# Kernel tuning notes

Hardware: AMD Instinct MI355X
Metric: run time of the kernel (lower is better)

Reference implementation:

```python
import jax, jax.numpy as jnp
import numpy as np

B, S, F_ATT, R, A = 1024, 96, 2048, 512, 512  # batch, att_size, att_feat_size, rnn_size, att_hid_size

def setup_inputs() -> dict:
    key = jax.random.key(0)
    ks = jax.random.split(key, 16)
    def lin(k, out_d, in_d):
        s = 1.0 / np.sqrt(in_d)
        kw, kb = jax.random.split(k)
        return (jax.random.uniform(kw, (out_d, in_d), jnp.float32, -s, s),
                jax.random.uniform(kb, (out_d,), jnp.float32, -s, s))
    W_ae, b_ae = lin(ks[0], R, F_ATT)   # att_embed Linear
    W_c,  b_c  = lin(ks[1], A, R)       # ctx2att
    W_s,  b_s  = lin(ks[2], A, R)       # sentinel_embed
    W_h,  b_h  = lin(ks[3], A, R)       # ho_embed
    W_al, b_al = lin(ks[4], 1, A)       # alpha_net
    W_o,  b_o  = lin(ks[5], R, R)       # att2h
    return {
        'h': jax.random.normal(ks[6], (B, R), jnp.float32),
        'sentinel': jax.random.normal(ks[7], (B, R), jnp.float32),
        'att_feats': jax.random.normal(ks[8], (B, S, F_ATT), jnp.float32),
        'W_ae': W_ae, 'b_ae': b_ae, 'W_c': W_c, 'b_c': b_c,
        'W_s': W_s, 'b_s': b_s, 'W_h': W_h, 'b_h': b_h,
        'W_al': W_al, 'b_al': b_al, 'W_o': W_o, 'b_o': b_o,
    }

def reference(h, sentinel, att_feats, W_ae, b_ae, W_c, b_c, W_s, b_s,
              W_h, b_h, W_al, b_al, W_o, b_o):
    # att_embed: Linear(2048->512) + ReLU (dropout = identity in eval)
    att = jax.nn.relu(jnp.einsum('bsf,rf->bsr', att_feats, W_ae) + b_ae)  # [B,S,R]
    att_embd = jnp.einsum('bsr,ar->bsa', att, W_c) + b_c                   # [B,S,A]
    sent_e = sentinel @ W_s.T + b_s                                        # [B,A]
    h_e = h @ W_h.T + b_h                                                  # [B,A]
    # concat sentinel slot in front of attention features
    img_all = jnp.concatenate([sentinel[:, None, :], att], axis=1)         # [B,S+1,R]
    img_all_embed = jnp.concatenate([sent_e[:, None, :], att_embd], axis=1)  # [B,S+1,A]
    hA = jnp.tanh(img_all_embed + h_e[:, None, :])                         # [B,S+1,A]
    logits = jnp.einsum('bsa,a->bs', hA, W_al[0]) + b_al[0]                # [B,S+1]
    alpha = jax.nn.softmax(logits, axis=-1)
    cHat = jnp.einsum('bs,bsr->br', alpha, img_all)                        # [B,R]
    atten_out = cHat + h
    return jnp.tanh(atten_out @ W_o.T + b_o)                               # [B,R]
```

## Files before the change

### kernel.cpp

```cpp
#include <hip/hip_runtime.h>

#define M1 98304
#define RDIM 512
#define FDIM 2048
#define SDIM 96
#define BM 96
#define BK 64

typedef __attribute__((ext_vector_type(8))) __bf16 bf16x8;
typedef __attribute__((ext_vector_type(4))) float f32x4;

#define WAITV6 asm volatile("s_waitcnt vmcnt(6)" ::: "memory")
#define WAITV3 asm volatile("s_waitcnt vmcnt(3)" ::: "memory")
#define WAITV0 asm volatile("s_waitcnt vmcnt(0)" ::: "memory")
#define WAITL0 asm volatile("s_waitcnt lgkmcnt(0)" ::: "memory")
#define SBAR   __builtin_amdgcn_s_barrier()
#define SCHED0 __builtin_amdgcn_sched_barrier(0)

__device__ __forceinline__ float bf2f(unsigned short u){
  union { unsigned int i; float f; } v; v.i = ((unsigned int)u) << 16; return v.f;
}
__device__ __forceinline__ unsigned short f2bf(float f){
  union { float f; unsigned int i; } v; v.f = f;
  unsigned int r = v.i + 0x7FFFu + ((v.i >> 16) & 1u);
  return (unsigned short)(r >> 16);
}
__device__ __forceinline__ unsigned short f2bfn(float f){
  __bf16 b = (__bf16)f;
  return __builtin_bit_cast(unsigned short, b);
}
__device__ __forceinline__ float fast_tanh(float x){
  float e = __expf(2.f * x);
  return 1.f - 2.f / (e + 1.f);
}
__device__ __forceinline__ void gld_lds16(const void* g, void* l){
  __builtin_amdgcn_global_load_lds((const __attribute__((address_space(1))) void*)g,
                                   (__attribute__((address_space(3))) void*)l, 16, 0, 0);
}
__device__ __forceinline__ f32x4 mfma16(bf16x8 a, bf16x8 b, f32x4 c){
  return __builtin_amdgcn_mfma_f32_16x16x32_bf16(a, b, c, 0, 0, 0);
}

__device__ __forceinline__ void cat_store_a(const float* __restrict__ src,
                                            unsigned short* __restrict__ dst, int idx){
  float x = src[idx];
  int r = idx >> 9, c = idx & 511;
  unsigned short hi = f2bf(x);
  unsigned short lo = f2bf(x - bf2f(hi));
  unsigned short* p = dst + (long)r * 1536 + c;
  p[0] = hi; p[512] = lo; p[1024] = hi;
}
__device__ __forceinline__ void cat_store_w(const float* __restrict__ src,
                                            unsigned short* __restrict__ dst, int idx){
  float x = src[idx];
  int r = idx >> 9, c = idx & 511;
  unsigned short hi = f2bf(x);
  unsigned short lo = f2bf(x - bf2f(hi));
  unsigned short* p = dst + (long)r * 1536 + c;
  p[0] = hi; p[512] = hi; p[1024] = lo;
}

__global__ void k_convert(const float* W_ae, const float* W_c, const float* W_s,
                          const float* W_h, const float* W_o,
                          const float* h, const float* sent,
                          unsigned short* W_ae_bf, unsigned short* W_c_bf,
                          unsigned short* W_s_cat, unsigned short* W_h_cat,
                          unsigned short* W_o_cat, unsigned short* h_cat,
                          unsigned short* s_cat){
  const int stride = 1024 * 256;
  int i0 = blockIdx.x * 256 + threadIdx.x;
  switch (blockIdx.y) {
    case 0: for (int i = i0; i < 512*2048; i += stride) W_ae_bf[i] = f2bf(W_ae[i]); break;
    case 1: for (int i = i0; i < 512*512;  i += stride) W_c_bf[i]  = f2bf(W_c[i]);  break;
    case 2: for (int i = i0; i < 512*512;  i += stride) cat_store_w(W_s, W_s_cat, i); break;
    case 3: for (int i = i0; i < 512*512;  i += stride) cat_store_w(W_h, W_h_cat, i); break;
    case 4: for (int i = i0; i < 512*512;  i += stride) cat_store_w(W_o, W_o_cat, i); break;
    case 5: for (int i = i0; i < 1024*512; i += stride) cat_store_a(h, h_cat, i); break;
    case 6: for (int i = i0; i < 1024*512; i += stride) cat_store_a(sent, s_cat, i); break;
  }
}

__global__ __launch_bounds__(512) void k_fused(
    const float* __restrict__ Af, const unsigned short* __restrict__ Wae,
    const float* __restrict__ b_ae,
    const unsigned short* __restrict__ Wcg, const float* __restrict__ b_c,
    const float* __restrict__ h_e, const float* __restrict__ W_al,
    const float* __restrict__ sent_e, const float* __restrict__ sent,
    const float* __restrict__ hvec, unsigned short* __restrict__ atten_cat){
  __shared__ __align__(16) char smem[155648];
  unsigned short* As   = (unsigned short*)smem;
  unsigned short* Bs   = (unsigned short*)(smem + 24576);
  unsigned short* attL = (unsigned short*)smem;
  unsigned short* Wcs  = (unsigned short*)(smem + 98304);
  float* part = (float*)(smem + 131072);
  float* lg   = (float*)(smem + 131072 + 1536);
  float* alp  = (float*)(smem + 131072 + 1536 + 512);
  float* ssum = (float*)(smem + 131072 + 1536 + 1024);

  const int tid = threadIdx.x;
  const int w = tid >> 6, l = tid & 63;
  const int wm = w >> 2, wn = w & 3;
  const int b = blockIdx.x;
  const long m0 = (long)b * BM;
  const int g = l >> 4, r15 = l & 15;
  const int rs = r15 & 7;

  f32x4 acc[3][8];
#pragma unroll
  for (int i = 0; i < 3; ++i)
#pragma unroll
    for (int j = 0; j < 8; ++j) acc[i][j] = f32x4{0.f,0.f,0.f,0.f};

  {
    const int brow_in = l >> 3;
    const int bswz = (l & 7) ^ brow_in;
    const unsigned short* bbase = Wae + (long)(w*64 + brow_in) * FDIM + bswz*8;
    int arow[3], akq[3], aswz[3];
    const float* abase[3];
#pragma unroll
    for (int s = 0; s < 3; ++s) {
      int c = tid + s*512;
      arow[s] = c >> 4; akq[s] = c & 15;
      abase[s] = Af + (m0 + arow[s])*FDIM + akq[s]*4;
      aswz[s] = arow[s]*BK + ((akq[s] ^ ((arow[s]&7)<<1))<<2);
    }
    const int NT = FDIM / BK;
    float4 d0,d1,d2, e0,e1,e2;
    float4 f0 = {0,0,0,0}, f1 = {0,0,0,0}, f2 = {0,0,0,0};

    {
      float4 c0 = *reinterpret_cast<const float4*>(abase[0]);
      float4 c1 = *reinterpret_cast<const float4*>(abase[1]);
      float4 c2 = *reinterpret_cast<const float4*>(abase[2]);
      SCHED0;
#pragma unroll
      for (int q = 0; q < 8; ++q)
        gld_lds16(bbase + (long)q*8*FDIM, Bs + (w*8+q)*512);
      SCHED0;
      d0 = *reinterpret_cast<const float4*>(abase[0] + BK);
      d1 = *reinterpret_cast<const float4*>(abase[1] + BK);
      d2 = *reinterpret_cast<const float4*>(abase[2] + BK);
      e0 = *reinterpret_cast<const float4*>(abase[0] + 2*BK);
      e1 = *reinterpret_cast<const float4*>(abase[1] + 2*BK);
      e2 = *reinterpret_cast<const float4*>(abase[2] + 2*BK);
      SCHED0;
      ushort4 p0; p0.x=f2bfn(c0.x); p0.y=f2bfn(c0.y); p0.z=f2bfn(c0.z); p0.w=f2bfn(c0.w);
      ushort4 p1; p1.x=f2bfn(c1.x); p1.y=f2bfn(c1.y); p1.z=f2bfn(c1.z); p1.w=f2bfn(c1.w);
      ushort4 p2; p2.x=f2bfn(c2.x); p2.y=f2bfn(c2.y); p2.z=f2bfn(c2.z); p2.w=f2bfn(c2.w);
      *reinterpret_cast<ushort4*>(&As[aswz[0]]) = p0;
      *reinterpret_cast<ushort4*>(&As[aswz[1]]) = p1;
      *reinterpret_cast<ushort4*>(&As[aswz[2]]) = p2;
      WAITV6; WAITL0; SCHED0; SBAR; SCHED0;
    }

    int cb = 0;
    for (int kt = 0; kt < NT; ++kt) {
      const int nb = cb ^ 1;
      if (kt + 1 < NT) {
        const int kof = (kt+1) * BK;
#pragma unroll
        for (int q = 0; q < 8; ++q)
          gld_lds16(bbase + (long)q*8*FDIM + kof, Bs + nb*32768 + (w*8+q)*512);
      }
      SCHED0;
      if (kt + 3 < NT) {
        const int kof = (kt+3) * BK;
        f0 = *reinterpret_cast<const float4*>(abase[0] + kof);
        f1 = *reinterpret_cast<const float4*>(abase[1] + kof);
        f2 = *reinterpret_cast<const float4*>(abase[2] + kof);
      }
      SCHED0;
#pragma unroll
      for (int hh = 0; hh < 2; ++hh) {
        const int ko = ((g + 4*hh) ^ rs) << 3;
        bf16x8 afr[3], bfr[8];
#pragma unroll
        for (int i = 0; i < 3; ++i)
          afr[i] = *reinterpret_cast<const bf16x8*>(&As[cb*6144 + (wm*48 + i*16 + r15)*BK + ko]);
#pragma unroll
        for (int j = 0; j < 8; ++j)
          bfr[j] = *reinterpret_cast<const bf16x8*>(&Bs[cb*32768 + (wn*128 + j*16 + r15)*BK + ko]);
        __builtin_amdgcn_s_setprio(1);
#pragma unroll
        for (int i = 0; i < 3; ++i)
#pragma unroll
          for (int j = 0; j < 8; ++j)
            acc[i][j] = mfma16(afr[i], bfr[j], acc[i][j]);
        __builtin_amdgcn_s_setprio(0);
      }
      if (kt + 1 < NT) {
        ushort4 p0; p0.x=f2bfn(d0.x); p0.y=f2bfn(d0.y); p0.z=f2bfn(d0.z); p0.w=f2bfn(d0.w);
        ushort4 p1; p1.x=f2bfn(d1.x); p1.y=f2bfn(d1.y); p1.z=f2bfn(d1.z); p1.w=f2bfn(d1.w);
        ushort4 p2; p2.x=f2bfn(d2.x); p2.y=f2bfn(d2.y); p2.z=f2bfn(d2.z); p2.w=f2bfn(d2.w);
        *reinterpret_cast<ushort4*>(&As[nb*6144 + aswz[0]]) = p0;
        *reinterpret_cast<ushort4*>(&As[nb*6144 + aswz[1]]) = p1;
        *reinterpret_cast<ushort4*>(&As[nb*6144 + aswz[2]]) = p2;
        d0=e0; d1=e1; d2=e2; e0=f0; e1=f1; e2=f2;
        if (kt + 3 < NT) { WAITV3; } else { WAITV0; }
        WAITL0; SCHED0; SBAR; SCHED0;
        cb = nb;
      }
    }
  }
  __syncthreads();
  {
    float bb[8];
#pragma unroll
    for (int j = 0; j < 8; ++j) bb[j] = b_ae[wn*128 + j*16 + r15];
#pragma unroll
    for (int i = 0; i < 3; ++i)
#pragma unroll
      for (int r = 0; r < 4; ++r) {
        int row = wm*48 + i*16 + g*4 + r;
        int rs8 = row & 7;
#pragma unroll
        for (int j = 0; j < 8; ++j) {
          int col = wn*128 + j*16 + r15;
          float x = acc[i][j][r] + bb[j];
          x = x > 0.f ? x : 0.f;
          attL[row*512 + (((col>>3) ^ rs8)<<3) + (col&7)] = f2bfn(x);
        }
      }
  }
  __syncthreads();

#pragma unroll
  for (int i = 0; i < 3; ++i)
#pragma unroll
    for (int j = 0; j < 8; ++j) acc[i][j] = f32x4{0.f,0.f,0.f,0.f};
  {
    const int crow = l >> 2;
    const int bsl2 = (l & 3) ^ ((l >> 3) & 3);
    const int rs2 = (r15 >> 1) & 3;
    uint4 rr0, rr1, rr2, rr3;
    rr0 = *reinterpret_cast<const uint4*>(Wcg + (long)(w*64 + 0*16 + crow)*RDIM + bsl2*8);
    rr1 = *reinterpret_cast<const uint4*>(Wcg + (long)(w*64 + 1*16 + crow)*RDIM + bsl2*8);
    rr2 = *reinterpret_cast<const uint4*>(Wcg + (long)(w*64 + 2*16 + crow)*RDIM + bsl2*8);
    rr3 = *reinterpret_cast<const uint4*>(Wcg + (long)(w*64 + 3*16 + crow)*RDIM + bsl2*8);
    for (int kt = 0; kt < 16; ++kt) {
      *reinterpret_cast<uint4*>(&Wcs[w*2048 + 0*512 + l*8]) = rr0;
      *reinterpret_cast<uint4*>(&Wcs[w*2048 + 1*512 + l*8]) = rr1;
      *reinterpret_cast<uint4*>(&Wcs[w*2048 + 2*512 + l*8]) = rr2;
      *reinterpret_cast<uint4*>(&Wcs[w*2048 + 3*512 + l*8]) = rr3;
      if (kt < 15) {
        const int k0 = (kt+1)*32;
        rr0 = *reinterpret_cast<const uint4*>(Wcg + (long)(w*64 + 0*16 + crow)*RDIM + k0 + bsl2*8);
        rr1 = *reinterpret_cast<const uint4*>(Wcg + (long)(w*64 + 1*16 + crow)*RDIM + k0 + bsl2*8);
        rr2 = *reinterpret_cast<const uint4*>(Wcg + (long)(w*64 + 2*16 + crow)*RDIM + k0 + bsl2*8);
        rr3 = *reinterpret_cast<const uint4*>(Wcg + (long)(w*64 + 3*16 + crow)*RDIM + k0 + bsl2*8);
      }
      WAITL0; SCHED0; SBAR; SCHED0;
      bf16x8 afr[3], bfr[8];
#pragma unroll
      for (int i = 0; i < 3; ++i) {
        int ra = wm*48 + i*16 + r15;
        int grp = (kt<<2) + g;
        afr[i] = *reinterpret_cast<const bf16x8*>(&attL[ra*512 + ((grp ^ rs)<<3)]);
      }
#pragma unroll
      for (int j = 0; j < 8; ++j)
        bfr[j] = *reinterpret_cast<const bf16x8*>(&Wcs[(wn*128 + j*16 + r15)*32 + ((g ^ rs2)<<3)]);
      __builtin_amdgcn_s_setprio(1);
#pragma unroll
      for (int i = 0; i < 3; ++i)
#pragma unroll
        for (int j = 0; j < 8; ++j)
          acc[i][j] = mfma16(afr[i], bfr[j], acc[i][j]);
      __builtin_amdgcn_s_setprio(0);
      WAITL0; SCHED0; SBAR; SCHED0;
    }
  }
  {
    const float* hrow = h_e + (long)b * RDIM;
    float bb2[8], wa[8], he[8];
#pragma unroll
    for (int j = 0; j < 8; ++j) {
      int n = wn*128 + j*16 + r15;
      bb2[j] = b_c[n]; wa[j] = W_al[n]; he[j] = hrow[n];
    }
#pragma unroll
    for (int i = 0; i < 3; ++i)
#pragma unroll
      for (int r = 0; r < 4; ++r) {
        int lrow = wm*48 + i*16 + g*4 + r;
        float s = 0.f;
#pragma unroll
        for (int j = 0; j < 8; ++j) {
          float x = acc[i][j][r] + bb2[j] + he[j];
          s += fast_tanh(x) * wa[j];
        }
        s += __shfl_xor(s, 1); s += __shfl_xor(s, 2);
        s += __shfl_xor(s, 4); s += __shfl_xor(s, 8);
        if (r15 == 0) part[lrow*4 + wn] = s;
      }
  }
  __syncthreads();
  if (tid < 96)
    lg[1+tid] = part[tid*4+0] + part[tid*4+1] + part[tid*4+2] + part[tid*4+3];
  if (tid < 64) {
    float s = 0.f;
    for (int a = tid; a < 512; a += 64)
      s += fast_tanh(sent_e[(long)b*512 + a] + h_e[(long)b*512 + a]) * W_al[a];
    s += __shfl_xor(s, 1); s += __shfl_xor(s, 2); s += __shfl_xor(s, 4);
    s += __shfl_xor(s, 8); s += __shfl_xor(s, 16); s += __shfl_xor(s, 32);
    if (tid == 0) lg[0] = s;
  }
  __syncthreads();
  if (tid < 64) {
    float m = -1e30f;
    for (int i = tid; i < 97; i += 64) m = fmaxf(m, lg[i]);
#pragma unroll
    for (int k = 1; k < 64; k <<= 1) m = fmaxf(m, __shfl_xor(m, k));
    float ss = 0.f;
    for (int i = tid; i < 97; i += 64) { float e = __expf(lg[i] - m); alp[i] = e; ss += e; }
#pragma unroll
    for (int k = 1; k < 64; k <<= 1) ss += __shfl_xor(ss, k);
    if (tid == 0) ssum[0] = ss;
  }
  __syncthreads();
  if (tid < 97) alp[tid] *= (1.f / ssum[0]);
  __syncthreads();
  {
    const int col = tid;
    const int cg = col >> 3, ch = col & 7;
    float accv = alp[0] * sent[(long)b*512 + col];
#pragma unroll 4
    for (int s = 0; s < SDIM; ++s)
      accv += alp[s+1] * bf2f(attL[s*512 + ((cg ^ (s&7))<<3) + ch]);
    float x = accv + hvec[(long)b*512 + col];
    unsigned short hi = f2bf(x);
    unsigned short lo = f2bf(x - bf2f(hi));
    unsigned short* pp = atten_cat + (long)b*1536 + col;
    pp[0] = hi; pp[512] = lo; pp[1024] = hi;
  }
}

__device__ __forceinline__ void small_gemm_body(
    const unsigned short* __restrict__ Abf, const unsigned short* __restrict__ Wb,
    const float* __restrict__ bias, float* __restrict__ Cout, int do_tanh, int bx,
    unsigned short* As, unsigned short* Bs){
  const int tid = threadIdx.x;
  const int w = tid >> 6, l = tid & 63;
  const int wm = w >> 1, wn = w & 1;
  const int m0 = (bx >> 3) * 64, n0 = (bx & 7) * 64;
  const int K = 1536;
  f32x4 acc[2][2];
#pragma unroll
  for (int i = 0; i < 2; ++i)
#pragma unroll
    for (int j = 0; j < 2; ++j) acc[i][j] = f32x4{0.f,0.f,0.f,0.f};

  const int crow = l >> 2;
  const int bsl = (l & 3) ^ ((l >> 3) & 3);
  const unsigned short* arow_p = Abf + (long)(m0 + w*16 + crow)*K + bsl*8;
  const unsigned short* brow_p = Wb  + (long)(n0 + w*16 + crow)*K + bsl*8;

  gld_lds16(arow_p, As + w*512);
  gld_lds16(brow_p, Bs + w*512);
  __syncthreads();
  int cb = 0;
  for (int kt = 0; kt < 48; ++kt) {
    const int nb = cb ^ 1;
    if (kt + 1 < 48) {
      const int k0 = (kt+1) * 32;
      gld_lds16(arow_p + k0, As + nb*2048 + w*512);
      gld_lds16(brow_p + k0, Bs + nb*2048 + w*512);
    }
    bf16x8 afr[2], bfr[2];
    const int g = l >> 4, r15 = l & 15;
    const int rs2 = (r15 >> 1) & 3;
#pragma unroll
    for (int i = 0; i < 2; ++i)
      afr[i] = *reinterpret_cast<const bf16x8*>(As + cb*2048 + (wm*32 + i*16 + r15)*32 + ((g ^ rs2)*8));
#pragma unroll
    for (int j = 0; j < 2; ++j)
      bfr[j] = *reinterpret_cast<const bf16x8*>(Bs + cb*2048 + (wn*32 + j*16 + r15)*32 + ((g ^ rs2)*8));
#pragma unroll
    for (int i = 0; i < 2; ++i)
#pragma unroll
      for (int j = 0; j < 2; ++j)
        acc[i][j] = mfma16(afr[i], bfr[j], acc[i][j]);
    if (kt + 1 < 48) { __syncthreads(); cb = nb; }
  }
  const int r15 = l & 15, g = l >> 4;
#pragma unroll
  for (int i = 0; i < 2; ++i)
#pragma unroll
    for (int r = 0; r < 4; ++r) {
      int m = m0 + wm*32 + i*16 + g*4 + r;
#pragma unroll
      for (int j = 0; j < 2; ++j) {
        int n = n0 + wn*32 + j*16 + r15;
        float x = acc[i][j][r] + bias[n];
        if (do_tanh) x = fast_tanh(x);
        Cout[(long)m * 512 + n] = x;
      }
    }
}

__global__ __launch_bounds__(256) void k_gemm_small(
    const unsigned short* __restrict__ Abf, const unsigned short* __restrict__ Wb,
    const float* __restrict__ bias, float* __restrict__ Cout, int do_tanh){
  __shared__ __align__(16) unsigned short As[2*64*32];
  __shared__ __align__(16) unsigned short Bs[2*64*32];
  small_gemm_body(Abf, Wb, bias, Cout, do_tanh, blockIdx.x, As, Bs);
}

__global__ __launch_bounds__(256) void k_embed2(
    const unsigned short* __restrict__ h_cat, const unsigned short* __restrict__ W_h_cat,
    const float* __restrict__ b_h, float* __restrict__ h_e,
    const unsigned short* __restrict__ s_cat, const unsigned short* __restrict__ W_s_cat,
    const float* __restrict__ b_s, float* __restrict__ sent_e){
  __shared__ __align__(16) unsigned short As[2*64*32];
  __shared__ __align__(16) unsigned short Bs[2*64*32];
  if (blockIdx.y == 0) small_gemm_body(h_cat, W_h_cat, b_h, h_e, 0, blockIdx.x, As, Bs);
  else                 small_gemm_body(s_cat, W_s_cat, b_s, sent_e, 0, blockIdx.x, As, Bs);
}

extern "C" void kernel_launch(void* const* d_in, const int* in_sizes, int n_in,
                              void* d_out, int out_size, void* d_ws, size_t ws_size,
                              hipStream_t stream){
  (void)in_sizes; (void)n_in; (void)out_size; (void)ws_size;
  const float* h    = (const float*)d_in[0];
  const float* sent = (const float*)d_in[1];
  const float* feats= (const float*)d_in[2];
  const float* W_ae = (const float*)d_in[3];
  const float* b_ae = (const float*)d_in[4];
  const float* W_c  = (const float*)d_in[5];
  const float* b_c  = (const float*)d_in[6];
  const float* W_s  = (const float*)d_in[7];
  const float* b_s  = (const float*)d_in[8];
  const float* W_h  = (const float*)d_in[9];
  const float* b_h  = (const float*)d_in[10];
  const float* W_al = (const float*)d_in[11];
  const float* W_o  = (const float*)d_in[13];
  const float* b_o  = (const float*)d_in[14];
  float* out = (float*)d_out;

  char* p = (char*)d_ws;
  unsigned short* W_ae_bf = (unsigned short*)p; p += (size_t)512*2048*2;
  unsigned short* W_c_bf  = (unsigned short*)p; p += (size_t)512*512*2;
  unsigned short* W_s_cat = (unsigned short*)p; p += (size_t)512*1536*2;
  unsigned short* W_h_cat = (unsigned short*)p; p += (size_t)512*1536*2;
  unsigned short* W_o_cat = (unsigned short*)p; p += (size_t)512*1536*2;
  unsigned short* h_cat   = (unsigned short*)p; p += (size_t)1024*1536*2;
  unsigned short* s_cat   = (unsigned short*)p; p += (size_t)1024*1536*2;
  unsigned short* at_cat  = (unsigned short*)p; p += (size_t)1024*1536*2;
  float* h_e    = (float*)p; p += (size_t)1024*512*4;
  float* sent_e = (float*)p; p += (size_t)1024*512*4;

  k_convert<<<dim3(1024,7), 256, 0, stream>>>(W_ae, W_c, W_s, W_h, W_o, h, sent,
        W_ae_bf, W_c_bf, W_s_cat, W_h_cat, W_o_cat, h_cat, s_cat);
  k_embed2<<<dim3(128,2), 256, 0, stream>>>(h_cat, W_h_cat, b_h, h_e,
                                            s_cat, W_s_cat, b_s, sent_e);
  k_fused<<<1024, 512, 0, stream>>>(feats, W_ae_bf, b_ae, W_c_bf, b_c,
                                    h_e, W_al, sent_e, sent, h, at_cat);
  k_gemm_small<<<128, 256, 0, stream>>>(at_cat, W_o_cat, b_o, out, 1);
}
```

Before: 416.5 us.

## Interleave B-tile global-to-LDS loads with the two MFMA k-halves using barriers

The main GEMM k-loop is restructured into two explicit half-steps. Each half issues half of the next B tile's global-to-LDS loads after its fragment reads, with the A prefetch moved into the second half. Extra workgroup barriers and lgkmcnt waits are added around each MFMA burst so waves move in lockstep, aiming to overlap memory issue with compute. The cost is two or three extra barriers per iteration, which may cause stalls.

```diff
diff --git a/kernel.cpp b/kernel.cpp
--- a/kernel.cpp
+++ b/kernel.cpp
@@ -115,14 +115,14 @@
     const int brow_in = l >> 3;
     const int bswz = (l & 7) ^ brow_in;
     const unsigned short* bbase = Wae + (long)(w*64 + brow_in) * FDIM + bswz*8;
-    int arow[3], akq[3], aswz[3];
+    int aswz[3];
     const float* abase[3];
 #pragma unroll
     for (int s = 0; s < 3; ++s) {
       int c = tid + s*512;
-      arow[s] = c >> 4; akq[s] = c & 15;
-      abase[s] = Af + (m0 + arow[s])*FDIM + akq[s]*4;
-      aswz[s] = arow[s]*BK + ((akq[s] ^ ((arow[s]&7)<<1))<<2);
+      int arow = c >> 4, akq = c & 15;
+      abase[s] = Af + (m0 + arow)*FDIM + akq*4;
+      aswz[s] = arow*BK + ((akq ^ ((arow&7)<<1))<<2);
     }
     const int NT = FDIM / BK;
     float4 d0,d1,d2, e0,e1,e2;
@@ -156,23 +156,11 @@
     int cb = 0;
     for (int kt = 0; kt < NT; ++kt) {
       const int nb = cb ^ 1;
-      if (kt + 1 < NT) {
-        const int kof = (kt+1) * BK;
-#pragma unroll
-        for (int q = 0; q < 8; ++q)
-          gld_lds16(bbase + (long)q*8*FDIM + kof, Bs + nb*32768 + (w*8+q)*512);
-      }
-      SCHED0;
-      if (kt + 3 < NT) {
-        const int kof = (kt+3) * BK;
-        f0 = *reinterpret_cast<const float4*>(abase[0] + kof);
-        f1 = *reinterpret_cast<const float4*>(abase[1] + kof);
-        f2 = *reinterpret_cast<const float4*>(abase[2] + kof);
-      }
-      SCHED0;
-#pragma unroll
-      for (int hh = 0; hh < 2; ++hh) {
-        const int ko = ((g + 4*hh) ^ rs) << 3;
+      const bool more = (kt + 1 < NT);
+      const long kof = (long)(kt+1) * BK;
+
+      {
+        const int ko = (g ^ rs) << 3;
         bf16x8 afr[3], bfr[8];
 #pragma unroll
         for (int i = 0; i < 3; ++i)
@@ -180,6 +168,13 @@
 #pragma unroll
         for (int j = 0; j < 8; ++j)
           bfr[j] = *reinterpret_cast<const bf16x8*>(&Bs[cb*32768 + (wn*128 + j*16 + r15)*BK + ko]);
+        if (more) {
+#pragma unroll
+          for (int q = 0; q < 4; ++q)
+            gld_lds16(bbase + (long)q*8*FDIM + kof, Bs + nb*32768 + (w*8+q)*512);
+        }
+        SCHED0; SBAR;
+        WAITL0; SCHED0;
         __builtin_amdgcn_s_setprio(1);
 #pragma unroll
         for (int i = 0; i < 3; ++i)
@@ -187,8 +182,40 @@
           for (int j = 0; j < 8; ++j)
             acc[i][j] = mfma16(afr[i], bfr[j], acc[i][j]);
         __builtin_amdgcn_s_setprio(0);
-      }
-      if (kt + 1 < NT) {
+        SCHED0; SBAR;
+      }
+      {
+        const int ko = ((g + 4) ^ rs) << 3;
+        bf16x8 afr[3], bfr[8];
+#pragma unroll
+        for (int i = 0; i < 3; ++i)
+          afr[i] = *reinterpret_cast<const bf16x8*>(&As[cb*6144 + (wm*48 + i*16 + r15)*BK + ko]);
+#pragma unroll
+        for (int j = 0; j < 8; ++j)
+          bfr[j] = *reinterpret_cast<const bf16x8*>(&Bs[cb*32768 + (wn*128 + j*16 + r15)*BK + ko]);
+        if (more) {
+#pragma unroll
+          for (int q = 4; q < 8; ++q)
+            gld_lds16(bbase + (long)q*8*FDIM + kof, Bs + nb*32768 + (w*8+q)*512);
+        }
+        SCHED0;
+        if (kt + 3 < NT) {
+          const long kof3 = (long)(kt+3) * BK;
+          f0 = *reinterpret_cast<const float4*>(abase[0] + kof3);
+          f1 = *reinterpret_cast<const float4*>(abase[1] + kof3);
+          f2 = *reinterpret_cast<const float4*>(abase[2] + kof3);
+        }
+        SCHED0; SBAR;
+        WAITL0; SCHED0;
+        __builtin_amdgcn_s_setprio(1);
+#pragma unroll
+        for (int i = 0; i < 3; ++i)
+#pragma unroll
+          for (int j = 0; j < 8; ++j)
+            acc[i][j] = mfma16(afr[i], bfr[j], acc[i][j]);
+        __builtin_amdgcn_s_setprio(0);
+      }
+      if (more) {
         ushort4 p0; p0.x=f2bfn(d0.x); p0.y=f2bfn(d0.y); p0.z=f2bfn(d0.z); p0.w=f2bfn(d0.w);
         ushort4 p1; p1.x=f2bfn(d1.x); p1.y=f2bfn(d1.y); p1.z=f2bfn(d1.z); p1.w=f2bfn(d1.w);
         ushort4 p2; p2.x=f2bfn(d2.x); p2.y=f2bfn(d2.y); p2.z=f2bfn(d2.z); p2.w=f2bfn(d2.w);
```

Result: slower. 448.9 us (+7.8%).
